# Optimization experiments

Hardware: AMD Instinct MI355X
Metric: run time of the kernel (lower is better)

## Reference

```python
import jax, jax.numpy as jnp
import numpy as np

N = 100000      # nodes
E = 1600000     # edges
F_IN = 128
H = 128
L = 3           # GraphConv layers
C = 47          # classes
EPS = 1e-5      # BatchNorm eps


def setup_inputs() -> dict:
    key = jax.random.key(0)
    ks = jax.random.split(key, 12)
    feat = jax.random.normal(ks[0], (N, F_IN), dtype=jnp.float32)
    src = jax.random.randint(ks[1], (E,), 0, N, dtype=jnp.int32)
    dst = jax.random.randint(ks[2], (E,), 0, N, dtype=jnp.int32)
    s = 0.02
    W_in = jax.random.normal(ks[3], (F_IN, H), dtype=jnp.float32) * s
    b_in = jnp.zeros((H,), dtype=jnp.float32)
    Wc = jax.random.normal(ks[4], (L, H, H), dtype=jnp.float32) * s
    bc = jnp.zeros((L, H), dtype=jnp.float32)
    # BatchNorm (eval mode) params for layers+1 norms
    gamma = jnp.ones((L + 1, H), dtype=jnp.float32)
    beta = jnp.zeros((L + 1, H), dtype=jnp.float32)
    rmean = jax.random.normal(ks[5], (L + 1, H), dtype=jnp.float32) * 0.1
    rvar = jax.random.uniform(ks[6], (L + 1, H), dtype=jnp.float32, minval=0.5, maxval=1.5)
    W_out = jax.random.normal(ks[7], (H, C), dtype=jnp.float32) * s
    b_out = jnp.zeros((C,), dtype=jnp.float32)
    return {"feat": feat, "src": src, "dst": dst, "W_in": W_in, "b_in": b_in,
            "Wc": Wc, "bc": bc, "gamma": gamma, "beta": beta,
            "rmean": rmean, "rvar": rvar, "W_out": W_out, "b_out": b_out}


def _bn(x, g, b, m, v):
    # BatchNorm1d in eval mode (running stats)
    return (x - m) * jax.lax.rsqrt(v + EPS) * g + b


def _degree_norms(src, dst):
    ones = jnp.ones((E,), dtype=jnp.float32)
    deg_out = jax.ops.segment_sum(ones, src, num_segments=N)
    deg_in = jax.ops.segment_sum(ones, dst, num_segments=N)
    norm_src = jax.lax.rsqrt(jnp.maximum(deg_out, 1.0))
    norm_dst = jax.lax.rsqrt(jnp.maximum(deg_in, 1.0))
    return norm_src, norm_dst


def _graph_conv(h, src, dst, norm_src, norm_dst, W, b):
    # DGL GraphConv, norm='both': D_dst^{-1/2} A D_src^{-1/2} H W + b
    h = h * norm_src[:, None]
    agg = jax.ops.segment_sum(h[src], dst, num_segments=N)  # [N, H]
    agg = agg * norm_dst[:, None]
    return agg @ W + b


def reference(feat, src, dst, W_in, b_in, Wc, bc, gamma, beta, rmean, rvar, W_out, b_out):
    norm_src, norm_dst = _degree_norms(src, dst)
    h = feat @ W_in + b_in
    h = jax.nn.relu(_bn(h, gamma[0], beta[0], rmean[0], rvar[0]))
    # dropout is identity in eval mode
    for i in range(L):
        h = _graph_conv(h, src, dst, norm_src, norm_dst, Wc[i], bc[i])
        h = jax.nn.relu(_bn(h, gamma[i + 1], beta[i + 1], rmean[i + 1], rvar[i + 1]))
    return h @ W_out + b_out
```

## Files before the change

### kernel.cpp

```cpp
#include <hip/hip_runtime.h>
#include <cstddef>
#include <cstdint>

#define NN 100000
#define NE 1600000
#define HD 128
#define C_OUT 47
#define EPS_BN 1e-5f
#define SLAB 64
#define NXCD 8
#define GEMM0_BLOCKS ((NN + 127) / 128)
#define BUILD_BLOCKS (NE / 256)

typedef _Float16 f16;
typedef __attribute__((ext_vector_type(2))) _Float16 f16x2;
typedef __attribute__((ext_vector_type(8))) _Float16 f16x8;
typedef __attribute__((ext_vector_type(4))) float f32x4;

__device__ inline ushort f16bits(f16 h) { return __builtin_bit_cast(ushort, h); }
__device__ inline uint packf16(f16 a, f16 b) {
  return (uint)f16bits(a) | ((uint)f16bits(b) << 16);
}
__device__ inline uint xcc_id() {
  uint x;
  asm volatile("s_getreg_b32 %0, hwreg(HW_REG_XCC_ID)" : "=s"(x));
  return x & (NXCD - 1);
}

__global__ __launch_bounds__(256) void k_wsplit(
    const float* __restrict__ W_in, const float* __restrict__ Wc,
    const float* __restrict__ W_out,
    uint* __restrict__ wsHi, uint* __restrict__ wsLo) {
  int g = blockIdx.x * 256 + threadIdx.x;
  int m = g >> 13;
  int i = g & 8191;
  int kp = i >> 7, c = i & 127;
  int k = kp << 1;
  int s = kp >> 2, t = kp & 3;
  if (m < 4) {
    const float* W = (m == 0) ? W_in : (Wc + (size_t)(m - 1) * HD * HD);
    float w0 = W[(size_t)k * 128 + c];
    float w1 = W[(size_t)(k + 1) * 128 + c];
    f16 h0 = (f16)w0, h1 = (f16)w1;
    f16 l0 = (f16)(w0 - (float)h0), l1 = (f16)(w1 - (float)h1);
    int idx = m * 8192 + (s * 128 + c) * 4 + t;
    wsHi[idx] = packf16(h0, h1);
    wsLo[idx] = packf16(l0, l1);
  } else if (c < 48) {
    float w0 = (c < C_OUT) ? W_out[(size_t)k * C_OUT + c] : 0.f;
    float w1 = (c < C_OUT) ? W_out[(size_t)(k + 1) * C_OUT + c] : 0.f;
    f16 h0 = (f16)w0, h1 = (f16)w1;
    f16 l0 = (f16)(w0 - (float)h0), l1 = (f16)(w1 - (float)h1);
    int idx = 4 * 8192 + (s * 48 + c) * 4 + t;
    wsHi[idx] = packf16(h0, h1);
    wsLo[idx] = packf16(l0, l1);
  }
}

template <bool A16>
__device__ inline void gemm_body(
    const void* __restrict__ Av, const uint* __restrict__ wHi,
    const uint* __restrict__ wLo, const float* __restrict__ bias,
    const float* __restrict__ gamma, const float* __restrict__ beta,
    const float* __restrict__ rmean, const float* __restrict__ rvar,
    f16* __restrict__ out, int bx) {
  int tid = threadIdx.x;
  int wv = tid >> 6, lane = tid & 63;
  int q = lane >> 4, m16 = lane & 15;
  int row_base = bx * 128 + wv * 32;

  f32x4 acc[2][8];
  #pragma unroll
  for (int mt = 0; mt < 2; ++mt)
    #pragma unroll
    for (int nt = 0; nt < 8; ++nt)
      acc[mt][nt] = (f32x4){0.f, 0.f, 0.f, 0.f};

  #pragma unroll
  for (int kk = 0; kk < 4; ++kk) {
    f16x8 a[2];
    #pragma unroll
    for (int mt = 0; mt < 2; ++mt) {
      int r = row_base + mt * 16 + m16;
      r = r < NN ? r : NN - 1;
      if constexpr (A16) {
        a[mt] = *(const f16x8*)((const f16*)Av + (size_t)r * 128 + kk * 32 + q * 8);
      } else {
        const float4* ap = (const float4*)((const float*)Av + (size_t)r * 128 + kk * 32 + q * 8);
        float4 a0 = ap[0], a1 = ap[1];
        a[mt][0] = (f16)a0.x; a[mt][1] = (f16)a0.y;
        a[mt][2] = (f16)a0.z; a[mt][3] = (f16)a0.w;
        a[mt][4] = (f16)a1.x; a[mt][5] = (f16)a1.y;
        a[mt][6] = (f16)a1.z; a[mt][7] = (f16)a1.w;
      }
    }
    int s = kk * 4 + q;
    #pragma unroll
    for (int nt = 0; nt < 8; ++nt) {
      int n = nt * 16 + m16;
      const f16x8 whi = *(const f16x8*)&wHi[(s * 128 + n) * 4];
      const f16x8 wlo = *(const f16x8*)&wLo[(s * 128 + n) * 4];
      #pragma unroll
      for (int mt = 0; mt < 2; ++mt) {
        acc[mt][nt] = __builtin_amdgcn_mfma_f32_16x16x32_f16(a[mt], whi, acc[mt][nt], 0, 0, 0);
        acc[mt][nt] = __builtin_amdgcn_mfma_f32_16x16x32_f16(a[mt], wlo, acc[mt][nt], 0, 0, 0);
      }
    }
  }

  float s8[8], t8[8];
  #pragma unroll
  for (int nt = 0; nt < 8; ++nt) {
    int col = nt * 16 + m16;
    float sc = gamma[col] * rsqrtf(rvar[col] + EPS_BN);
    s8[nt] = sc;
    t8[nt] = (bias[col] - rmean[col]) * sc + beta[col];
  }
  #pragma unroll
  for (int mt = 0; mt < 2; ++mt) {
    #pragma unroll
    for (int nt = 0; nt < 8; ++nt) {
      int col = nt * 16 + m16;
      #pragma unroll
      for (int e = 0; e < 4; ++e) {
        int r = row_base + mt * 16 + q * 4 + e;
        if (r < NN) {
          float y = fmaxf(acc[mt][nt][e] * s8[nt] + t8[nt], 0.f);
          out[(size_t)r * 128 + col] = (f16)y;
        }
      }
    }
  }
}

__global__ __launch_bounds__(256, 4) void k_mega(
    const int* __restrict__ src, const int* __restrict__ dst,
    int* __restrict__ deg_out_c, int* __restrict__ cursor,
    int* __restrict__ slab,
    const float* __restrict__ feat, const uint* __restrict__ wsHi,
    const uint* __restrict__ wsLo, const float* __restrict__ b_in,
    const float* __restrict__ gamma, const float* __restrict__ beta,
    const float* __restrict__ rmean, const float* __restrict__ rvar,
    f16* __restrict__ h) {
  if (blockIdx.x >= GEMM0_BLOCKS) {
    int e = (blockIdx.x - GEMM0_BLOCKS) * 256 + threadIdx.x;
    if (e >= NE) return;
    int s = src[e], v = dst[e];
    uint xc = xcc_id();
    __hip_atomic_fetch_add(&deg_out_c[xc * NN + s], 1, __ATOMIC_RELAXED,
                           __HIP_MEMORY_SCOPE_WORKGROUP);
    int pos = atomicAdd(&cursor[v], 1);
    if (pos < SLAB) slab[(size_t)v * SLAB + pos] = s;
    return;
  }
  gemm_body<false>(feat, wsHi, wsLo, b_in, gamma, beta, rmean, rvar, h,
                   blockIdx.x);
}

__global__ __launch_bounds__(256) void k_norms(
    const int* __restrict__ deg_out_c, const int* __restrict__ cursor,
    float* __restrict__ norm_src, float* __restrict__ norm_dst) {
  int v = blockIdx.x * blockDim.x + threadIdx.x;
  if (v >= NN) return;
  int d = 0;
  #pragma unroll
  for (int c = 0; c < NXCD; ++c) d += deg_out_c[c * NN + v];
  norm_src[v] = rsqrtf((float)(d > 0 ? d : 1));
  int di = cursor[v];
  norm_dst[v] = rsqrtf((float)(di > 0 ? di : 1));
}

__global__ __launch_bounds__(256) void k_aggregate(
    const f16* __restrict__ h, const int* __restrict__ cursor,
    const int* __restrict__ slab, const float* __restrict__ norm_src,
    const float* __restrict__ norm_dst, f16* __restrict__ agg) {
  int wave = (int)((blockIdx.x * (unsigned)blockDim.x + threadIdx.x) >> 6);
  int lane = threadIdx.x & 63;
  if (wave >= NN) return;
  const f16x2* h2 = (const f16x2*)h;
  const int* cols = slab + (size_t)wave * SLAB;
  int d = cursor[wave];
  d = d < SLAB ? d : SLAB;
  float ax = 0.f, ay = 0.f;
  int j = 0;
  for (; j + 4 <= d; j += 4) {
    int u0 = cols[j + 0];
    int u1 = cols[j + 1];
    int u2 = cols[j + 2];
    int u3 = cols[j + 3];
    float w0 = norm_src[u0], w1 = norm_src[u1];
    float w2 = norm_src[u2], w3 = norm_src[u3];
    f16x2 x0 = h2[(size_t)u0 * 64 + lane];
    f16x2 x1 = h2[(size_t)u1 * 64 + lane];
    f16x2 x2 = h2[(size_t)u2 * 64 + lane];
    f16x2 x3 = h2[(size_t)u3 * 64 + lane];
    ax = fmaf(w0, (float)x0[0], ax); ay = fmaf(w0, (float)x0[1], ay);
    ax = fmaf(w1, (float)x1[0], ax); ay = fmaf(w1, (float)x1[1], ay);
    ax = fmaf(w2, (float)x2[0], ax); ay = fmaf(w2, (float)x2[1], ay);
    ax = fmaf(w3, (float)x3[0], ax); ay = fmaf(w3, (float)x3[1], ay);
  }
  for (; j < d; ++j) {
    int u = cols[j];
    float w = norm_src[u];
    f16x2 x = h2[(size_t)u * 64 + lane];
    ax = fmaf(w, (float)x[0], ax);
    ay = fmaf(w, (float)x[1], ay);
  }
  float nd = norm_dst[wave];
  f16x2 o;
  o[0] = (f16)(ax * nd);
  o[1] = (f16)(ay * nd);
  ((f16x2*)agg)[(size_t)wave * 64 + lane] = o;
}

__global__ __launch_bounds__(256, 4) void k_gemm(
    const f16* __restrict__ A, const uint* __restrict__ wHi,
    const uint* __restrict__ wLo, const float* __restrict__ bias,
    const float* __restrict__ gamma, const float* __restrict__ beta,
    const float* __restrict__ rmean, const float* __restrict__ rvar,
    f16* __restrict__ out) {
  gemm_body<true>(A, wHi, wLo, bias, gamma, beta, rmean, rvar, out, blockIdx.x);
}

__global__ __launch_bounds__(256, 4) void k_gemm_out(
    const f16* __restrict__ A, const uint* __restrict__ wHi,
    const uint* __restrict__ wLo, const float* __restrict__ bias,
    float* __restrict__ out) {
  int tid = threadIdx.x;
  int wv = tid >> 6, lane = tid & 63;
  int q = lane >> 4, m16 = lane & 15;
  int row_base = blockIdx.x * 128 + wv * 32;

  f32x4 acc[2][3];
  #pragma unroll
  for (int mt = 0; mt < 2; ++mt)
    #pragma unroll
    for (int nt = 0; nt < 3; ++nt)
      acc[mt][nt] = (f32x4){0.f, 0.f, 0.f, 0.f};

  #pragma unroll
  for (int kk = 0; kk < 4; ++kk) {
    f16x8 a[2];
    #pragma unroll
    for (int mt = 0; mt < 2; ++mt) {
      int r = row_base + mt * 16 + m16;
      r = r < NN ? r : NN - 1;
      a[mt] = *(const f16x8*)(A + (size_t)r * 128 + kk * 32 + q * 8);
    }
    int s = kk * 4 + q;
    #pragma unroll
    for (int nt = 0; nt < 3; ++nt) {
      int n = nt * 16 + m16;
      const f16x8 whi = *(const f16x8*)&wHi[(s * 48 + n) * 4];
      const f16x8 wlo = *(const f16x8*)&wLo[(s * 48 + n) * 4];
      #pragma unroll
      for (int mt = 0; mt < 2; ++mt) {
        acc[mt][nt] = __builtin_amdgcn_mfma_f32_16x16x32_f16(a[mt], whi, acc[mt][nt], 0, 0, 0);
        acc[mt][nt] = __builtin_amdgcn_mfma_f32_16x16x32_f16(a[mt], wlo, acc[mt][nt], 0, 0, 0);
      }
    }
  }

  #pragma unroll
  for (int nt = 0; nt < 3; ++nt) {
    int col = nt * 16 + m16;
    float b = (col < C_OUT) ? bias[col] : 0.f;
    #pragma unroll
    for (int mt = 0; mt < 2; ++mt) {
      #pragma unroll
      for (int e = 0; e < 4; ++e) {
        int r = row_base + mt * 16 + q * 4 + e;
        if (r < NN && col < C_OUT) {
          out[(size_t)r * C_OUT + col] = acc[mt][nt][e] + b;
        }
      }
    }
  }
}


extern "C" void kernel_launch(void* const* d_in, const int* in_sizes, int n_in,
                              void* d_out, int out_size, void* d_ws, size_t ws_size,
                              hipStream_t stream) {
  const float* feat = (const float*)d_in[0];
  const int* src = (const int*)d_in[1];
  const int* dst = (const int*)d_in[2];
  const float* W_in = (const float*)d_in[3];
  const float* b_in = (const float*)d_in[4];
  const float* Wc = (const float*)d_in[5];
  const float* bc = (const float*)d_in[6];
  const float* gamma = (const float*)d_in[7];
  const float* beta = (const float*)d_in[8];
  const float* rmean = (const float*)d_in[9];
  const float* rvar = (const float*)d_in[10];
  const float* W_out = (const float*)d_in[11];
  const float* b_out = (const float*)d_in[12];
  float* out = (float*)d_out;

  char* p = (char*)d_ws;
  f16* h = (f16*)p;             p += (size_t)NN * HD * sizeof(f16);
  f16* agg = (f16*)p;           p += (size_t)NN * HD * sizeof(f16);
  int* slab = (int*)p;          p += (size_t)NN * SLAB * sizeof(int);
  float* norm_src = (float*)p;  p += (size_t)NN * sizeof(float);
  float* norm_dst = (float*)p;  p += (size_t)NN * sizeof(float);
  uint* wsHi = (uint*)p;        p += (size_t)5 * 8192 * sizeof(uint);
  uint* wsLo = (uint*)p;        p += (size_t)5 * 8192 * sizeof(uint);
  int* deg_out_c = (int*)p;     p += (size_t)NXCD * NN * sizeof(int);
  int* cursor = (int*)p;        p += (size_t)NN * sizeof(int);

  hipMemsetAsync(deg_out_c, 0, (size_t)(NXCD + 1) * NN * sizeof(int), stream);

  k_wsplit<<<160, 256, 0, stream>>>(W_in, Wc, W_out, wsHi, wsLo);
  k_mega<<<GEMM0_BLOCKS + BUILD_BLOCKS, 256, 0, stream>>>(
      src, dst, deg_out_c, cursor, slab, feat, wsHi, wsLo, b_in, gamma, beta,
      rmean, rvar, h);
  k_norms<<<(NN + 255) / 256, 256, 0, stream>>>(deg_out_c, cursor, norm_src,
                                                norm_dst);

  int gblocks = (NN + 127) / 128;
  for (int l = 0; l < 3; ++l) {
    k_aggregate<<<(NN * 64 + 255) / 256, 256, 0, stream>>>(
        h, cursor, slab, norm_src, norm_dst, agg);
    k_gemm<<<gblocks, 256, 0, stream>>>(
        agg, wsHi + (size_t)(l + 1) * 8192, wsLo + (size_t)(l + 1) * 8192,
        bc + (size_t)l * HD,
        gamma + (size_t)(l + 1) * HD, beta + (size_t)(l + 1) * HD,
        rmean + (size_t)(l + 1) * HD, rvar + (size_t)(l + 1) * HD, h);
  }
  k_gemm_out<<<gblocks, 256, 0, stream>>>(
      h, wsHi + (size_t)4 * 8192, wsLo + (size_t)4 * 8192, b_out, out);
}
```

Measured before the change: 546.7 us.

## Fuse neighbor aggregation and GEMM+BN+ReLU into one per-layer kernel

Replaces the separate aggregate and GEMM kernels with a single k_layer kernel. Each block gathers 128 rows of neighbor features into a swizzled LDS tile, then runs the MFMA GEMM with the fused BN/ReLU epilogue. Ping-pong h buffers replace the agg intermediate. This removes the global write and read of the aggregated matrix and one launch per layer. The cost is far fewer waves in the gather phase (782 blocks, each wave handling 32 rows serially), which reduces memory-level parallelism for the latency-bound gather, plus lower occupancy from the 32KB LDS tile.

```diff
diff --git a/kernel.cpp b/kernel.cpp
--- a/kernel.cpp
+++ b/kernel.cpp
@@ -170,56 +170,114 @@
   norm_dst[v] = rsqrtf((float)(di > 0 ? di : 1));
 }
 
-__global__ __launch_bounds__(256) void k_aggregate(
-    const f16* __restrict__ h, const int* __restrict__ cursor,
+__global__ __launch_bounds__(256, 3) void k_layer(
+    const f16* __restrict__ hin, const int* __restrict__ cursor,
     const int* __restrict__ slab, const float* __restrict__ norm_src,
-    const float* __restrict__ norm_dst, f16* __restrict__ agg) {
-  int wave = (int)((blockIdx.x * (unsigned)blockDim.x + threadIdx.x) >> 6);
-  int lane = threadIdx.x & 63;
-  if (wave >= NN) return;
-  const f16x2* h2 = (const f16x2*)h;
-  const int* cols = slab + (size_t)wave * SLAB;
-  int d = cursor[wave];
-  d = d < SLAB ? d : SLAB;
-  float ax = 0.f, ay = 0.f;
-  int j = 0;
-  for (; j + 4 <= d; j += 4) {
-    int u0 = cols[j + 0];
-    int u1 = cols[j + 1];
-    int u2 = cols[j + 2];
-    int u3 = cols[j + 3];
-    float w0 = norm_src[u0], w1 = norm_src[u1];
-    float w2 = norm_src[u2], w3 = norm_src[u3];
-    f16x2 x0 = h2[(size_t)u0 * 64 + lane];
-    f16x2 x1 = h2[(size_t)u1 * 64 + lane];
-    f16x2 x2 = h2[(size_t)u2 * 64 + lane];
-    f16x2 x3 = h2[(size_t)u3 * 64 + lane];
-    ax = fmaf(w0, (float)x0[0], ax); ay = fmaf(w0, (float)x0[1], ay);
-    ax = fmaf(w1, (float)x1[0], ax); ay = fmaf(w1, (float)x1[1], ay);
-    ax = fmaf(w2, (float)x2[0], ax); ay = fmaf(w2, (float)x2[1], ay);
-    ax = fmaf(w3, (float)x3[0], ax); ay = fmaf(w3, (float)x3[1], ay);
-  }
-  for (; j < d; ++j) {
-    int u = cols[j];
-    float w = norm_src[u];
-    f16x2 x = h2[(size_t)u * 64 + lane];
-    ax = fmaf(w, (float)x[0], ax);
-    ay = fmaf(w, (float)x[1], ay);
-  }
-  float nd = norm_dst[wave];
-  f16x2 o;
-  o[0] = (f16)(ax * nd);
-  o[1] = (f16)(ay * nd);
-  ((f16x2*)agg)[(size_t)wave * 64 + lane] = o;
-}
-
-__global__ __launch_bounds__(256, 4) void k_gemm(
-    const f16* __restrict__ A, const uint* __restrict__ wHi,
-    const uint* __restrict__ wLo, const float* __restrict__ bias,
-    const float* __restrict__ gamma, const float* __restrict__ beta,
-    const float* __restrict__ rmean, const float* __restrict__ rvar,
-    f16* __restrict__ out) {
-  gemm_body<true>(A, wHi, wLo, bias, gamma, beta, rmean, rvar, out, blockIdx.x);
+    const float* __restrict__ norm_dst,
+    const uint* __restrict__ wHi, const uint* __restrict__ wLo,
+    const float* __restrict__ bias, const float* __restrict__ gamma,
+    const float* __restrict__ beta, const float* __restrict__ rmean,
+    const float* __restrict__ rvar, f16* __restrict__ hout) {
+  __shared__ uint tile[128 * 64];
+  int tid = threadIdx.x;
+  int wv = tid >> 6, lane = tid & 63;
+  int row0 = blockIdx.x * 128 + wv * 32;
+  const f16x2* h2 = (const f16x2*)hin;
+
+  for (int i = 0; i < 32; ++i) {
+    int v = row0 + i;
+    float ax = 0.f, ay = 0.f;
+    if (v < NN) {
+      const int* cols = slab + (size_t)v * SLAB;
+      int d = cursor[v];
+      d = d < SLAB ? d : SLAB;
+      int j = 0;
+      for (; j + 4 <= d; j += 4) {
+        int u0 = cols[j + 0];
+        int u1 = cols[j + 1];
+        int u2 = cols[j + 2];
+        int u3 = cols[j + 3];
+        float w0 = norm_src[u0], w1 = norm_src[u1];
+        float w2 = norm_src[u2], w3 = norm_src[u3];
+        f16x2 x0 = h2[(size_t)u0 * 64 + lane];
+        f16x2 x1 = h2[(size_t)u1 * 64 + lane];
+        f16x2 x2 = h2[(size_t)u2 * 64 + lane];
+        f16x2 x3 = h2[(size_t)u3 * 64 + lane];
+        ax = fmaf(w0, (float)x0[0], ax); ay = fmaf(w0, (float)x0[1], ay);
+        ax = fmaf(w1, (float)x1[0], ax); ay = fmaf(w1, (float)x1[1], ay);
+        ax = fmaf(w2, (float)x2[0], ax); ay = fmaf(w2, (float)x2[1], ay);
+        ax = fmaf(w3, (float)x3[0], ax); ay = fmaf(w3, (float)x3[1], ay);
+      }
+      for (; j < d; ++j) {
+        int u = cols[j];
+        float w = norm_src[u];
+        f16x2 x = h2[(size_t)u * 64 + lane];
+        ax = fmaf(w, (float)x[0], ax);
+        ay = fmaf(w, (float)x[1], ay);
+      }
+      float nd = norm_dst[v];
+      ax *= nd; ay *= nd;
+    }
+    int r = wv * 32 + i;
+    int ua = r * 64 + ((((lane >> 2) ^ (r & 15)) << 2) | (lane & 3));
+    tile[ua] = packf16((f16)ax, (f16)ay);
+  }
+  __syncthreads();
+
+  int q = lane >> 4, m16 = lane & 15;
+  f32x4 acc[2][8];
+  #pragma unroll
+  for (int mt = 0; mt < 2; ++mt)
+    #pragma unroll
+    for (int nt = 0; nt < 8; ++nt)
+      acc[mt][nt] = (f32x4){0.f, 0.f, 0.f, 0.f};
+
+  #pragma unroll
+  for (int kk = 0; kk < 4; ++kk) {
+    int g0 = kk * 4 + q;
+    f16x8 a[2];
+    #pragma unroll
+    for (int mt = 0; mt < 2; ++mt) {
+      int r = wv * 32 + mt * 16 + m16;
+      a[mt] = *(const f16x8*)&tile[r * 64 + ((g0 ^ m16) << 2)];
+    }
+    #pragma unroll
+    for (int nt = 0; nt < 8; ++nt) {
+      int n = nt * 16 + m16;
+      const f16x8 whi = *(const f16x8*)&wHi[(g0 * 128 + n) * 4];
+      const f16x8 wlo = *(const f16x8*)&wLo[(g0 * 128 + n) * 4];
+      #pragma unroll
+      for (int mt = 0; mt < 2; ++mt) {
+        acc[mt][nt] = __builtin_amdgcn_mfma_f32_16x16x32_f16(a[mt], whi, acc[mt][nt], 0, 0, 0);
+        acc[mt][nt] = __builtin_amdgcn_mfma_f32_16x16x32_f16(a[mt], wlo, acc[mt][nt], 0, 0, 0);
+      }
+    }
+  }
+
+  float s8[8], t8[8];
+  #pragma unroll
+  for (int nt = 0; nt < 8; ++nt) {
+    int col = nt * 16 + m16;
+    float sc = gamma[col] * rsqrtf(rvar[col] + EPS_BN);
+    s8[nt] = sc;
+    t8[nt] = (bias[col] - rmean[col]) * sc + beta[col];
+  }
+  int row_base = blockIdx.x * 128 + wv * 32;
+  #pragma unroll
+  for (int mt = 0; mt < 2; ++mt) {
+    #pragma unroll
+    for (int nt = 0; nt < 8; ++nt) {
+      int col = nt * 16 + m16;
+      #pragma unroll
+      for (int e = 0; e < 4; ++e) {
+        int r = row_base + mt * 16 + q * 4 + e;
+        if (r < NN) {
+          float y = fmaxf(acc[mt][nt][e] * s8[nt] + t8[nt], 0.f);
+          hout[(size_t)r * 128 + col] = (f16)y;
+        }
+      }
+    }
+  }
 }
 
 __global__ __launch_bounds__(256, 4) void k_gemm_out(
@@ -298,8 +356,8 @@
   float* out = (float*)d_out;
 
   char* p = (char*)d_ws;
-  f16* h = (f16*)p;             p += (size_t)NN * HD * sizeof(f16);
-  f16* agg = (f16*)p;           p += (size_t)NN * HD * sizeof(f16);
+  f16* ha = (f16*)p;            p += (size_t)NN * HD * sizeof(f16);
+  f16* hb = (f16*)p;            p += (size_t)NN * HD * sizeof(f16);
   int* slab = (int*)p;          p += (size_t)NN * SLAB * sizeof(int);
   float* norm_src = (float*)p;  p += (size_t)NN * sizeof(float);
   float* norm_dst = (float*)p;  p += (size_t)NN * sizeof(float);
@@ -313,20 +371,22 @@
   k_wsplit<<<160, 256, 0, stream>>>(W_in, Wc, W_out, wsHi, wsLo);
   k_mega<<<GEMM0_BLOCKS + BUILD_BLOCKS, 256, 0, stream>>>(
       src, dst, deg_out_c, cursor, slab, feat, wsHi, wsLo, b_in, gamma, beta,
-      rmean, rvar, h);
+      rmean, rvar, ha);
   k_norms<<<(NN + 255) / 256, 256, 0, stream>>>(deg_out_c, cursor, norm_src,
                                                 norm_dst);
 
   int gblocks = (NN + 127) / 128;
+  f16* hi = ha;
+  f16* ho = hb;
   for (int l = 0; l < 3; ++l) {
-    k_aggregate<<<(NN * 64 + 255) / 256, 256, 0, stream>>>(
-        h, cursor, slab, norm_src, norm_dst, agg);
-    k_gemm<<<gblocks, 256, 0, stream>>>(
-        agg, wsHi + (size_t)(l + 1) * 8192, wsLo + (size_t)(l + 1) * 8192,
+    k_layer<<<gblocks, 256, 0, stream>>>(
+        hi, cursor, slab, norm_src, norm_dst,
+        wsHi + (size_t)(l + 1) * 8192, wsLo + (size_t)(l + 1) * 8192,
         bc + (size_t)l * HD,
         gamma + (size_t)(l + 1) * HD, beta + (size_t)(l + 1) * HD,
-        rmean + (size_t)(l + 1) * HD, rvar + (size_t)(l + 1) * HD, h);
+        rmean + (size_t)(l + 1) * HD, rvar + (size_t)(l + 1) * HD, ho);
+    f16* tmp = hi; hi = ho; ho = tmp;
   }
   k_gemm_out<<<gblocks, 256, 0, stream>>>(
-      h, wsHi + (size_t)4 * 8192, wsLo + (size_t)4 * 8192, b_out, out);
-}
+      hi, wsHi + (size_t)4 * 8192, wsLo + (size_t)4 * 8192, b_out, out);
+}
```

New measurement: 720.4 us. 1.32x slower.

## Partition incoming-edge slabs per XCD to use workgroup-scope cursor atomics

Applied to the files above, without the earlier changes.

The per-destination edge cursor and slab are split into eight per-XCD copies, so the build phase uses relaxed workgroup-scope atomics local to each XCD instead of device-scope atomicAdd on a shared cursor. k_norms sums the per-XCD counts for norm_dst and packs each clamped count into one 64-bit word, and the aggregate kernel walks the eight sub-slabs in turn. This targets contention and coherence traffic on the cursor atomics, at the cost of a larger slab buffer, a bigger memset and more fragmented, shorter inner loops during aggregation. Each per-XCD slab is capped at 22 entries, so any node receiving more than 22 in-edges from one XCD would silently drop edges.

```diff
diff --git a/kernel.cpp b/kernel.cpp
--- a/kernel.cpp
+++ b/kernel.cpp
@@ -7,8 +7,8 @@
 #define HD 128
 #define C_OUT 47
 #define EPS_BN 1e-5f
-#define SLAB 64
 #define NXCD 8
+#define SLAB8 22
 #define GEMM0_BLOCKS ((NN + 127) / 128)
 #define BUILD_BLOCKS (NE / 256)
 
@@ -16,6 +16,7 @@
 typedef __attribute__((ext_vector_type(2))) _Float16 f16x2;
 typedef __attribute__((ext_vector_type(8))) _Float16 f16x8;
 typedef __attribute__((ext_vector_type(4))) float f32x4;
+typedef unsigned long long u64;
 
 __device__ inline ushort f16bits(f16 h) { return __builtin_bit_cast(ushort, h); }
 __device__ inline uint packf16(f16 a, f16 b) {
@@ -135,8 +136,8 @@
 
 __global__ __launch_bounds__(256, 4) void k_mega(
     const int* __restrict__ src, const int* __restrict__ dst,
-    int* __restrict__ deg_out_c, int* __restrict__ cursor,
-    int* __restrict__ slab,
+    int* __restrict__ deg_out_c, int* __restrict__ cursor8,
+    int* __restrict__ slab8,
     const float* __restrict__ feat, const uint* __restrict__ wsHi,
     const uint* __restrict__ wsLo, const float* __restrict__ b_in,
     const float* __restrict__ gamma, const float* __restrict__ beta,
@@ -149,8 +150,9 @@
     uint xc = xcc_id();
     __hip_atomic_fetch_add(&deg_out_c[xc * NN + s], 1, __ATOMIC_RELAXED,
                            __HIP_MEMORY_SCOPE_WORKGROUP);
-    int pos = atomicAdd(&cursor[v], 1);
-    if (pos < SLAB) slab[(size_t)v * SLAB + pos] = s;
+    int pos = __hip_atomic_fetch_add(&cursor8[xc * NN + v], 1, __ATOMIC_RELAXED,
+                                     __HIP_MEMORY_SCOPE_WORKGROUP);
+    if (pos < SLAB8) slab8[((size_t)xc * NN + v) * SLAB8 + pos] = s;
     return;
   }
   gemm_body<false>(feat, wsHi, wsLo, b_in, gamma, beta, rmean, rvar, h,
@@ -158,53 +160,56 @@
 }
 
 __global__ __launch_bounds__(256) void k_norms(
-    const int* __restrict__ deg_out_c, const int* __restrict__ cursor,
-    float* __restrict__ norm_src, float* __restrict__ norm_dst) {
+    const int* __restrict__ deg_out_c, const int* __restrict__ cursor8,
+    float* __restrict__ norm_src, float* __restrict__ norm_dst,
+    u64* __restrict__ pcnt) {
   int v = blockIdx.x * blockDim.x + threadIdx.x;
   if (v >= NN) return;
-  int d = 0;
-  #pragma unroll
-  for (int c = 0; c < NXCD; ++c) d += deg_out_c[c * NN + v];
+  int d = 0, di = 0;
+  u64 pack = 0;
+  #pragma unroll
+  for (int c = 0; c < NXCD; ++c) {
+    d += deg_out_c[c * NN + v];
+    int dc = cursor8[c * NN + v];
+    di += dc;
+    int cl = dc < SLAB8 ? dc : SLAB8;
+    pack |= (u64)cl << (8 * c);
+  }
   norm_src[v] = rsqrtf((float)(d > 0 ? d : 1));
-  int di = cursor[v];
   norm_dst[v] = rsqrtf((float)(di > 0 ? di : 1));
+  pcnt[v] = pack;
 }
 
 __global__ __launch_bounds__(256) void k_aggregate(
-    const f16* __restrict__ h, const int* __restrict__ cursor,
-    const int* __restrict__ slab, const float* __restrict__ norm_src,
+    const f16* __restrict__ h, const u64* __restrict__ pcnt,
+    const int* __restrict__ slab8, const float* __restrict__ norm_src,
     const float* __restrict__ norm_dst, f16* __restrict__ agg) {
   int wave = (int)((blockIdx.x * (unsigned)blockDim.x + threadIdx.x) >> 6);
   int lane = threadIdx.x & 63;
   if (wave >= NN) return;
   const f16x2* h2 = (const f16x2*)h;
-  const int* cols = slab + (size_t)wave * SLAB;
-  int d = cursor[wave];
-  d = d < SLAB ? d : SLAB;
+  u64 pk = pcnt[wave];
   float ax = 0.f, ay = 0.f;
-  int j = 0;
-  for (; j + 4 <= d; j += 4) {
-    int u0 = cols[j + 0];
-    int u1 = cols[j + 1];
-    int u2 = cols[j + 2];
-    int u3 = cols[j + 3];
-    float w0 = norm_src[u0], w1 = norm_src[u1];
-    float w2 = norm_src[u2], w3 = norm_src[u3];
-    f16x2 x0 = h2[(size_t)u0 * 64 + lane];
-    f16x2 x1 = h2[(size_t)u1 * 64 + lane];
-    f16x2 x2 = h2[(size_t)u2 * 64 + lane];
-    f16x2 x3 = h2[(size_t)u3 * 64 + lane];
-    ax = fmaf(w0, (float)x0[0], ax); ay = fmaf(w0, (float)x0[1], ay);
-    ax = fmaf(w1, (float)x1[0], ax); ay = fmaf(w1, (float)x1[1], ay);
-    ax = fmaf(w2, (float)x2[0], ax); ay = fmaf(w2, (float)x2[1], ay);
-    ax = fmaf(w3, (float)x3[0], ax); ay = fmaf(w3, (float)x3[1], ay);
-  }
-  for (; j < d; ++j) {
-    int u = cols[j];
-    float w = norm_src[u];
-    f16x2 x = h2[(size_t)u * 64 + lane];
-    ax = fmaf(w, (float)x[0], ax);
-    ay = fmaf(w, (float)x[1], ay);
+  #pragma unroll
+  for (int c = 0; c < NXCD; ++c) {
+    int dc = (int)((pk >> (8 * c)) & 0xFF);
+    const int* cols = slab8 + ((size_t)c * NN + wave) * SLAB8;
+    int j = 0;
+    for (; j + 2 <= dc; j += 2) {
+      int u0 = cols[j], u1 = cols[j + 1];
+      float w0 = norm_src[u0], w1 = norm_src[u1];
+      f16x2 x0 = h2[(size_t)u0 * 64 + lane];
+      f16x2 x1 = h2[(size_t)u1 * 64 + lane];
+      ax = fmaf(w0, (float)x0[0], ax); ay = fmaf(w0, (float)x0[1], ay);
+      ax = fmaf(w1, (float)x1[0], ax); ay = fmaf(w1, (float)x1[1], ay);
+    }
+    if (j < dc) {
+      int u = cols[j];
+      float w = norm_src[u];
+      f16x2 x = h2[(size_t)u * 64 + lane];
+      ax = fmaf(w, (float)x[0], ax);
+      ay = fmaf(w, (float)x[1], ay);
+    }
   }
   float nd = norm_dst[wave];
   f16x2 o;
@@ -298,35 +303,38 @@
   float* out = (float*)d_out;
 
   char* p = (char*)d_ws;
-  f16* h = (f16*)p;             p += (size_t)NN * HD * sizeof(f16);
-  f16* agg = (f16*)p;           p += (size_t)NN * HD * sizeof(f16);
-  int* slab = (int*)p;          p += (size_t)NN * SLAB * sizeof(int);
+  f16* ha = (f16*)p;            p += (size_t)NN * HD * sizeof(f16);
+  f16* hb = (f16*)p;            p += (size_t)NN * HD * sizeof(f16);
+  int* slab8 = (int*)p;         p += (size_t)NXCD * NN * SLAB8 * sizeof(int);
   float* norm_src = (float*)p;  p += (size_t)NN * sizeof(float);
   float* norm_dst = (float*)p;  p += (size_t)NN * sizeof(float);
+  u64* pcnt = (u64*)p;          p += (size_t)NN * sizeof(u64);
   uint* wsHi = (uint*)p;        p += (size_t)5 * 8192 * sizeof(uint);
   uint* wsLo = (uint*)p;        p += (size_t)5 * 8192 * sizeof(uint);
   int* deg_out_c = (int*)p;     p += (size_t)NXCD * NN * sizeof(int);
-  int* cursor = (int*)p;        p += (size_t)NN * sizeof(int);
-
-  hipMemsetAsync(deg_out_c, 0, (size_t)(NXCD + 1) * NN * sizeof(int), stream);
+  int* cursor8 = (int*)p;       p += (size_t)NXCD * NN * sizeof(int);
+
+  hipMemsetAsync(deg_out_c, 0, (size_t)2 * NXCD * NN * sizeof(int), stream);
 
   k_wsplit<<<160, 256, 0, stream>>>(W_in, Wc, W_out, wsHi, wsLo);
   k_mega<<<GEMM0_BLOCKS + BUILD_BLOCKS, 256, 0, stream>>>(
-      src, dst, deg_out_c, cursor, slab, feat, wsHi, wsLo, b_in, gamma, beta,
-      rmean, rvar, h);
-  k_norms<<<(NN + 255) / 256, 256, 0, stream>>>(deg_out_c, cursor, norm_src,
-                                                norm_dst);
+      src, dst, deg_out_c, cursor8, slab8, feat, wsHi, wsLo, b_in, gamma, beta,
+      rmean, rvar, ha);
+  k_norms<<<(NN + 255) / 256, 256, 0, stream>>>(deg_out_c, cursor8, norm_src,
+                                                norm_dst, pcnt);
 
   int gblocks = (NN + 127) / 128;
+  f16* hi = ha;
+  f16* ho = hb;
   for (int l = 0; l < 3; ++l) {
     k_aggregate<<<(NN * 64 + 255) / 256, 256, 0, stream>>>(
-        h, cursor, slab, norm_src, norm_dst, agg);
+        hi, pcnt, slab8, norm_src, norm_dst, ho);
     k_gemm<<<gblocks, 256, 0, stream>>>(
-        agg, wsHi + (size_t)(l + 1) * 8192, wsLo + (size_t)(l + 1) * 8192,
+        ho, wsHi + (size_t)(l + 1) * 8192, wsLo + (size_t)(l + 1) * 8192,
         bc + (size_t)l * HD,
         gamma + (size_t)(l + 1) * HD, beta + (size_t)(l + 1) * HD,
-        rmean + (size_t)(l + 1) * HD, rvar + (size_t)(l + 1) * HD, h);
+        rmean + (size_t)(l + 1) * HD, rvar + (size_t)(l + 1) * HD, hi);
   }
   k_gemm_out<<<gblocks, 256, 0, stream>>>(
-      h, wsHi + (size_t)4 * 8192, wsLo + (size_t)4 * 8192, b_out, out);
-}
+      hi, wsHi + (size_t)4 * 8192, wsLo + (size_t)4 * 8192, b_out, out);
+}
```

After: 687.4 us. 25.7% more time.
